# Kernel tuning notes

Hardware: AMD Instinct MI355X
Metric: run time of the kernel (lower is better)

The kernel has to match this reference:

```python
import jax, jax.numpy as jnp
import numpy as np
from jax import lax

K = 5          # CARAFE kernel_size
S = 2          # scale_factor (downsample stride)
GROUP = 1      # mask groups
ENC_PAD = 1    # (encoder_kernel-1)*dilation//2 with encoder_kernel=3


def _conv2d(x, w, b, stride, padding, dilation=1):
    y = lax.conv_general_dilated(
        x, w, window_strides=(stride, stride),
        padding=[(padding, padding), (padding, padding)],
        rhs_dilation=(dilation, dilation),
        dimension_numbers=('NCHW', 'OIHW', 'NCHW'))
    return y + b[None, :, None, None]


def setup_inputs() -> dict:
    key = jax.random.key(0)
    k1, k2, k3 = jax.random.split(key, 3)
    B, C, H, W = 4, 256, 128, 128
    COMP = 64
    x = jax.random.normal(k1, (B, C, H, W), dtype=jnp.float32)
    # xavier-uniform-ish scale for compressor, std=0.001 for content encoder (as in init_weights)
    w1 = jax.random.normal(k2, (COMP, C, 1, 1), dtype=jnp.float32) * (1.0 / np.sqrt(C))
    b1 = jnp.zeros((COMP,), dtype=jnp.float32)
    w2 = jax.random.normal(k3, (K * K * GROUP, COMP, 3, 3), dtype=jnp.float32) * 0.001
    b2 = jnp.zeros((K * K * GROUP,), dtype=jnp.float32)
    return {"x": x, "w1": w1, "b1": b1, "w2": w2, "b2": b2}


def _carafe_forward(x, w1, b1, w2, b2):
    B, C, H, W = x.shape
    compressed = _conv2d(x, w1, b1, stride=1, padding=0)           # (B, 64, H, W)
    mask = _conv2d(compressed, w2, b2, stride=S, padding=ENC_PAD)   # (B, K*K*G, Ho, Wo)
    Ho, Wo = mask.shape[2], mask.shape[3]
    # kernel_normalizer: softmax over the K*K window per group
    mask = jax.nn.softmax(mask.reshape(B, GROUP, K * K, Ho, Wo), axis=2)
    # feature_reassemble: fused unfold * mask sum — accumulate per kernel tap to
    # avoid materializing the full (B, C, K*K, Ho, Wo) tensor.
    pad = K // 2
    x_pad = jnp.pad(x, ((0, 0), (0, 0), (pad, pad), (pad, pad)))
    Cg = C // GROUP
    out = jnp.zeros((B, GROUP, Cg, Ho, Wo), dtype=x.dtype)
    for i in range(K):
        for j in range(K):
            patch = x_pad[:, :, i:i + S * (Ho - 1) + 1:S, j:j + S * (Wo - 1) + 1:S]
            patch = patch.reshape(B, GROUP, Cg, Ho, Wo)
            out = out + patch * mask[:, :, i * K + j][:, :, None]
    return out.reshape(B, C, Ho, Wo)


def reference(x, w1, b1, w2, b2):
    return _carafe_forward(x, w1, b1, w2, b2)
```

## Files before the change

### kernel.cpp

```cpp
#include <hip/hip_runtime.h>
#include <math.h>

#define BN   4
#define CN   256
#define HN   128
#define WN   128
#define COMP 64
#define KK   25
#define HO   64
#define WO   64

#define TB_OFF    36864
#define WS_NEED   ((size_t)(TB_OFF + 256) * 4)

typedef short v8s  __attribute__((ext_vector_type(8)));
typedef float v16f __attribute__((ext_vector_type(16)));

__device__ inline ushort f2bf(float f) {
  unsigned u = __float_as_uint(f);
  return (ushort)((u + 0x7fffu + ((u >> 16) & 1u)) >> 16);
}

__global__ __launch_bounds__(256) void compose_kernel(
    const float* __restrict__ w1, const float* __restrict__ b1,
    const float* __restrict__ w2, float* __restrict__ ws) {
  const int cid = blockIdx.x;
  const int tid = threadIdx.x;
  const int t = cid >> 2;
  const int chunk = (cid & 3) * 4 + (tid >> 6);
  const int lane = tid & 63;
  const int m = lane & 31, half = lane >> 5;
  const int c0 = chunk * 16 + half * 8;
  float acc[8] = {0.f, 0.f, 0.f, 0.f, 0.f, 0.f, 0.f, 0.f};
  if (m < KK) {
    for (int k = 0; k < COMP; ++k) {
      float wv = w2[(size_t)(m * COMP + k) * 9 + t];
      const float* w1r = w1 + (size_t)k * CN + c0;
      float4 a = *(const float4*)w1r;
      float4 bq = *(const float4*)(w1r + 4);
      acc[0] += wv * a.x;  acc[1] += wv * a.y;
      acc[2] += wv * a.z;  acc[3] += wv * a.w;
      acc[4] += wv * bq.x; acc[5] += wv * bq.y;
      acc[6] += wv * bq.z; acc[7] += wv * bq.w;
    }
  }
  ushort* wA = (ushort*)ws;
  ushort pk[8];
#pragma unroll
  for (int j = 0; j < 8; ++j) pk[j] = f2bf(acc[j]);
  *(ushort4*)(wA + ((size_t)(t * 16 + chunk) * 64 + lane) * 8) =
      make_ushort4(pk[0], pk[1], pk[2], pk[3]);
  *(ushort4*)(wA + ((size_t)(t * 16 + chunk) * 64 + lane) * 8 + 4) =
      make_ushort4(pk[4], pk[5], pk[6], pk[7]);
  if (chunk == 0 && lane < KK) {
    float tbv = 0.f;
    for (int k = 0; k < COMP; ++k)
      tbv += w2[(size_t)(lane * COMP + k) * 9 + t] * b1[k];
    ws[TB_OFF + lane * 9 + t] = tbv;
  }
}

__global__ __launch_bounds__(1024, 4) void fused_main(
    const float* __restrict__ ws, const float* __restrict__ b2,
    const float* __restrict__ x, float* __restrict__ out) {
  const int ho = blockIdx.x, b = blockIdx.y;
  const int tid = threadIdx.x;
  const int lane = tid & 63;
  const int wv = tid >> 6;
  const int n = lane & 31, half = lane >> 5;

  __shared__ __attribute__((aligned(16))) char smem[57600];
  float* red = (float*)smem;
  float* sml = (float*)(smem + 51200);

  const ushort* wA = (const ushort*)ws;
  const float* __restrict__ xb = x + (size_t)(b * CN) * (HN * WN);

  const int px = tid & 127;
  const int cg = tid >> 7;
  float sreg[3][8];

  auto stage_load = [&](int c) {
#pragma unroll
    for (int dr = 0; dr < 3; ++dr) {
      const int r = 2 * ho + dr - 1;
      if (r >= 0) {
        const float* xp = xb + ((size_t)(c * 64 + cg * 8) * HN + r) * WN + px;
#pragma unroll
        for (int i = 0; i < 8; ++i) sreg[dr][i] = xp[(size_t)i * (HN * WN)];
      } else {
#pragma unroll
        for (int i = 0; i < 8; ++i) sreg[dr][i] = 0.f;
      }
    }
  };
  auto stage_write = [&]() {
#pragma unroll
    for (int dr = 0; dr < 3; ++dr) {
      v8s o;
#pragma unroll
      for (int i = 0; i < 8; ++i) o[i] = (short)f2bf(sreg[dr][i]);
      const int boff = (((dr * 128 + px) * 64 + cg * 8) * 2)
                       ^ (((px >> 1) & 7) << 4);
      *(v8s*)(smem + boff) = o;
    }
  };

  const int kf = wv & 3;
  const int tg = wv >> 2;
  const v8s zero8 = {};
  v16f acc[2] = {{}, {}};

  stage_load(0);
  for (int c = 0; c < 4; ++c) {
    __syncthreads();
    stage_write();
    __syncthreads();
    if (c < 3) stage_load(c + 1);
    const int kidx = c * 4 + kf;
#pragma unroll
    for (int t = 0; t < 9; ++t) {
      const int tgt = (t >= 6) ? 3 : (t >> 1);
      if (tgt != tg) continue;
      const int dr = t / 3, dc = t % 3;
      if (2 * ho + dr - 1 < 0) continue;
      const v8s af = *(const v8s*)(wA + ((size_t)(t * 16 + kidx) * 64 + lane) * 8);
#pragma unroll
      for (int wt = 0; wt < 2; ++wt) {
        const int q = 2 * (wt * 32 + n) + dc - 1;
        const bool bad = q < 0;
        const int qc = bad ? 0 : q;
        const int boff = (((dr * 128 + qc) * 64 + kf * 16 + half * 8) * 2)
                         ^ (((qc >> 1) & 7) << 4);
        v8s bf = *(const v8s*)(smem + boff);
        if (dc == 0 && bad) bf = zero8;
        acc[wt] = __builtin_amdgcn_mfma_f32_32x32x16_bf16(af, bf, acc[wt], 0, 0, 0);
      }
    }
  }

  const int wo = lane;
  const int c_base = __builtin_amdgcn_readfirstlane(wv * 16);
  const int col = 2 * wo;
  float2 g[2][5];
  auto load_g = [&](int ci, float2* dst) {
    const float* xc = xb + (size_t)(c_base + ci) * (HN * WN);
#pragma unroll
    for (int i = 0; i < 5; ++i) {
      int r = 2 * ho - 2 + i;
      dst[i] = (r >= 0 && r < HN) ? *(const float2*)(xc + r * WN + col)
                                  : make_float2(0.f, 0.f);
    }
  };
  load_g(0, g[0]);
  load_g(1, g[1]);

  __syncthreads();

  if (wv >= 8) {
#pragma unroll
    for (int wt = 0; wt < 2; ++wt)
#pragma unroll
      for (int rg = 0; rg < 16; ++rg) {
        int m = (rg & 3) + 8 * (rg >> 2) + 4 * half;
        if (m < KK) red[((wv - 8) * KK + m) * 64 + wt * 32 + n] = acc[wt][rg];
      }
  }
  __syncthreads();
  if (wv < 8) {
#pragma unroll
    for (int wt = 0; wt < 2; ++wt)
#pragma unroll
      for (int rg = 0; rg < 16; ++rg) {
        int m = (rg & 3) + 8 * (rg >> 2) + 4 * half;
        if (m < KK) red[(wv * KK + m) * 64 + wt * 32 + n] += acc[wt][rg];
      }
  }
  __syncthreads();
  if (wv < 4) {
#pragma unroll
    for (int m = 0; m < KK; ++m)
      red[(wv * KK + m) * 64 + wo] += red[((wv + 4) * KK + m) * 64 + wo];
  }
  __syncthreads();
  if (wv < 2) {
#pragma unroll
    for (int m = 0; m < KK; ++m)
      red[(wv * KK + m) * 64 + wo] += red[((wv + 2) * KK + m) * 64 + wo];
  }
  __syncthreads();
  if (tid < 64) {
    const float* tb = ws + TB_OFF;
    const float vr0 = (ho > 0) ? 1.f : 0.f;
    const float vq0 = (wo > 0) ? 1.f : 0.f;
    float logit[KK];
    float mx = -1e30f;
#pragma unroll
    for (int m = 0; m < KK; ++m) {
      const float* t9 = tb + m * 9;
      float l = b2[m]
              + vr0 * (vq0 * t9[0] + t9[1] + t9[2])
              +       (vq0 * t9[3] + t9[4] + t9[5])
              +       (vq0 * t9[6] + t9[7] + t9[8]);
      l += red[(0 * KK + m) * 64 + wo] + red[(1 * KK + m) * 64 + wo];
      logit[m] = l;
      mx = fmaxf(mx, l);
    }
    float ssum = 0.f;
#pragma unroll
    for (int m = 0; m < KK; ++m) {
      float e = __expf(logit[m] - mx);
      logit[m] = e;
      ssum += e;
    }
    float inv = 1.f / ssum;
#pragma unroll
    for (int m = 0; m < KK; ++m) sml[m * 64 + wo] = logit[m] * inv;
  }
  __syncthreads();

  float smr[KK];
#pragma unroll
  for (int m = 0; m < KK; ++m) smr[m] = sml[m * 64 + wo];

  const float wok = (wo > 0) ? 1.f : 0.f;
  const float w63 = (wo < 63) ? 1.f : 0.f;
  for (int ci = 0; ci < 16; ++ci) {
    float2 v[5];
#pragma unroll
    for (int i = 0; i < 5; ++i) v[i] = g[ci & 1][i];
    if (ci + 2 < 16) load_g(ci + 2, g[ci & 1]);

    float acc2 = 0.f;
#pragma unroll
    for (int i = 0; i < 5; ++i) {
      float lx = wok * __shfl_up(v[i].x, 1, 64);
      float ly = wok * __shfl_up(v[i].y, 1, 64);
      float rx = w63 * __shfl_down(v[i].x, 1, 64);
      acc2 += lx * smr[i * 5 + 0] + ly * smr[i * 5 + 1]
            + v[i].x * smr[i * 5 + 2] + v[i].y * smr[i * 5 + 3]
            + rx * smr[i * 5 + 4];
    }
    out[(((size_t)(b * CN + c_base + ci)) * HO + ho) * WO + wo] = acc2;
  }
}

#define FB_WSTRIDE 240
#define FB_TB_OFF  (256 * FB_WSTRIDE)

__global__ __launch_bounds__(256) void compose_w_fb(
    const float* __restrict__ w1, const float* __restrict__ b1,
    const float* __restrict__ w2, float* __restrict__ ws) {
  int mt = blockIdx.x, c = threadIdx.x;
  float acc = 0.f;
#pragma unroll 8
  for (int k = 0; k < COMP; ++k)
    acc += w2[(size_t)(mt / 9 * COMP + k) * 9 + (mt % 9)] * w1[k * CN + c];
  ws[c * FB_WSTRIDE + mt] = acc;
  if (mt < FB_WSTRIDE - 225) ws[c * FB_WSTRIDE + 225 + mt] = 0.f;
  if (c == 0) {
    float tbv = 0.f;
    for (int k = 0; k < COMP; ++k)
      tbv += w2[(size_t)(mt / 9 * COMP + k) * 9 + (mt % 9)] * b1[k];
    ws[FB_TB_OFF + mt] = tbv;
  }
}

__global__ __launch_bounds__(1024, 4) void fused_fb(
    const float* __restrict__ x, const float* __restrict__ b2,
    const float* __restrict__ ws, float* __restrict__ out) {
  const int ho = blockIdx.x, b = blockIdx.y, tid = threadIdx.x;
  const int wo = tid & 63, wv = tid >> 6;
  const int c_base = __builtin_amdgcn_readfirstlane(wv * 16);
  const float* __restrict__ w2c = ws;
  const float* __restrict__ tb  = ws + FB_TB_OFF;
  __shared__ float red[8 * KK * 64];
  __shared__ float sm[KK * 64];
  const float* __restrict__ xb = x + (size_t)(b * CN) * (HN * WN);
  const int col = 2 * wo;
  float acc[KK];
#pragma unroll
  for (int m = 0; m < KK; ++m) acc[m] = 0.f;
  float2 xbuf[2][3];
  auto load_ch = [&](int ci, float2* dst) {
    const float* xc = xb + (size_t)(c_base + ci) * (HN * WN);
    dst[0] = (ho > 0) ? *(const float2*)(xc + (2 * ho - 1) * WN + col)
                      : make_float2(0.f, 0.f);
    dst[1] = *(const float2*)(xc + (2 * ho) * WN + col);
    dst[2] = *(const float2*)(xc + (2 * ho + 1) * WN + col);
  };
  load_ch(0, xbuf[0]);
  load_ch(1, xbuf[1]);
  const float wok = (wo > 0) ? 1.f : 0.f;
  for (int ci = 0; ci < 16; ++ci) {
    float2 r0 = xbuf[ci & 1][0], r1 = xbuf[ci & 1][1], r2 = xbuf[ci & 1][2];
    if (ci + 2 < 16) load_ch(ci + 2, xbuf[ci & 1]);
    float xv[9];
    xv[0] = wok * __shfl_up(r0.y, 1, 64); xv[1] = r0.x; xv[2] = r0.y;
    xv[3] = wok * __shfl_up(r1.y, 1, 64); xv[4] = r1.x; xv[5] = r1.y;
    xv[6] = wok * __shfl_up(r2.y, 1, 64); xv[7] = r2.x; xv[8] = r2.y;
    const float* __restrict__ wrow = w2c + (size_t)(c_base + ci) * FB_WSTRIDE;
#pragma unroll
    for (int m = 0; m < KK; ++m) {
      float a = acc[m];
#pragma unroll
      for (int t = 0; t < 9; ++t) a += wrow[m * 9 + t] * xv[t];
      acc[m] = a;
    }
  }
  float2 g[2][5];
  auto load_g = [&](int ci, float2* dst) {
    const float* xc = xb + (size_t)(c_base + ci) * (HN * WN);
#pragma unroll
    for (int i = 0; i < 5; ++i) {
      int r = 2 * ho - 2 + i;
      dst[i] = (r >= 0 && r < HN) ? *(const float2*)(xc + r * WN + col)
                                  : make_float2(0.f, 0.f);
    }
  };
  load_g(0, g[0]);
  load_g(1, g[1]);
  if (wv >= 8) {
#pragma unroll
    for (int m = 0; m < KK; ++m) red[((wv - 8) * KK + m) * 64 + wo] = acc[m];
  }
  __syncthreads();
  if (wv < 8) {
#pragma unroll
    for (int m = 0; m < KK; ++m) red[(wv * KK + m) * 64 + wo] += acc[m];
  }
  __syncthreads();
  if (wv < 4) {
#pragma unroll
    for (int m = 0; m < KK; ++m)
      red[(wv * KK + m) * 64 + wo] += red[((wv + 4) * KK + m) * 64 + wo];
  }
  __syncthreads();
  if (wv < 2) {
#pragma unroll
    for (int m = 0; m < KK; ++m)
      red[(wv * KK + m) * 64 + wo] += red[((wv + 2) * KK + m) * 64 + wo];
  }
  __syncthreads();
  if (tid < 64) {
    const float vr0 = (ho > 0) ? 1.f : 0.f;
    const float vq0 = (wo > 0) ? 1.f : 0.f;
    float logit[KK];
    float mx = -1e30f;
#pragma unroll
    for (int m = 0; m < KK; ++m) {
      const float* t9 = tb + m * 9;
      float l = b2[m]
              + vr0 * (vq0 * t9[0] + t9[1] + t9[2])
              +       (vq0 * t9[3] + t9[4] + t9[5])
              +       (vq0 * t9[6] + t9[7] + t9[8]);
      l += red[(0 * KK + m) * 64 + wo] + red[(1 * KK + m) * 64 + wo];
      logit[m] = l;
      mx = fmaxf(mx, l);
    }
    float s = 0.f;
#pragma unroll
    for (int m = 0; m < KK; ++m) {
      float e = __expf(logit[m] - mx);
      logit[m] = e;
      s += e;
    }
    float inv = 1.f / s;
#pragma unroll
    for (int m = 0; m < KK; ++m) sm[m * 64 + wo] = logit[m] * inv;
  }
  __syncthreads();
  float smr[KK];
#pragma unroll
  for (int m = 0; m < KK; ++m) smr[m] = sm[m * 64 + wo];
  const float w63 = (wo < 63) ? 1.f : 0.f;
  for (int ci = 0; ci < 16; ++ci) {
    float2 v[5];
#pragma unroll
    for (int i = 0; i < 5; ++i) v[i] = g[ci & 1][i];
    if (ci + 2 < 16) load_g(ci + 2, g[ci & 1]);
    float acc2 = 0.f;
#pragma unroll
    for (int i = 0; i < 5; ++i) {
      float lx = wok * __shfl_up(v[i].x, 1, 64);
      float ly = wok * __shfl_up(v[i].y, 1, 64);
      float rx = w63 * __shfl_down(v[i].x, 1, 64);
      acc2 += lx * smr[i * 5 + 0] + ly * smr[i * 5 + 1]
            + v[i].x * smr[i * 5 + 2] + v[i].y * smr[i * 5 + 3]
            + rx * smr[i * 5 + 4];
    }
    out[(((size_t)(b * CN + c_base + ci)) * HO + ho) * WO + wo] = acc2;
  }
}

extern "C" void kernel_launch(void* const* d_in, const int* in_sizes, int n_in,
                              void* d_out, int out_size, void* d_ws, size_t ws_size,
                              hipStream_t stream) {
  const float* x  = (const float*)d_in[0];
  const float* w1 = (const float*)d_in[1];
  const float* b1 = (const float*)d_in[2];
  const float* w2 = (const float*)d_in[3];
  const float* b2 = (const float*)d_in[4];
  float* out = (float*)d_out;
  float* ws  = (float*)d_ws;

  if (ws_size >= WS_NEED) {
    hipLaunchKernelGGL(compose_kernel, dim3(36), dim3(256), 0, stream,
                       w1, b1, w2, ws);
    hipLaunchKernelGGL(fused_main, dim3(HO, BN), dim3(1024), 0, stream,
                       ws, b2, x, out);
  } else {
    hipLaunchKernelGGL(compose_w_fb, dim3(225), dim3(256), 0, stream,
                       w1, b1, w2, ws);
    hipLaunchKernelGGL(fused_fb, dim3(HO, BN), dim3(1024), 0, stream,
                       x, b2, ws, out);
  }
}
```

Before: 149.0 us.

## Split fused CARAFE kernel into channel-split conv partials and softmax-gather kernel

The single fused kernel, which ran 256 blocks each looping over four channel chunks, becomes two kernels. The first computes per-chunk partial mask logits across a 4x larger grid and writes them to workspace. The second sums the four partials, applies softmax, and reassembles a quarter of the output channels per block. This raises block count and occupancy and removes the serial channel loop. In exchange it adds a global round-trip for partial logits, an extra launch, and redundant softmax work in each of the four channel-quarter blocks.

```diff
diff --git a/kernel.cpp b/kernel.cpp
--- a/kernel.cpp
+++ b/kernel.cpp
@@ -11,7 +11,9 @@
 #define WO   64
 
 #define TB_OFF    36864
-#define WS_NEED   ((size_t)(TB_OFF + 256) * 4)
+#define P_OFF     37120
+#define P_COUNT   ((size_t)BN * HO * 4 * KK * 64)
+#define WS_NEED   ((size_t)(P_OFF + P_COUNT) * 4)
 
 typedef short v8s  __attribute__((ext_vector_type(8)));
 typedef float v16f __attribute__((ext_vector_type(16)));
@@ -60,18 +62,16 @@
   }
 }
 
-__global__ __launch_bounds__(1024, 4) void fused_main(
-    const float* __restrict__ ws, const float* __restrict__ b2,
-    const float* __restrict__ x, float* __restrict__ out) {
-  const int ho = blockIdx.x, b = blockIdx.y;
+__global__ __launch_bounds__(1024, 8) void conv_partial(
+    float* __restrict__ ws, const float* __restrict__ x) {
+  const int ho = blockIdx.x, b = blockIdx.y, cq = blockIdx.z;
   const int tid = threadIdx.x;
   const int lane = tid & 63;
   const int wv = tid >> 6;
   const int n = lane & 31, half = lane >> 5;
 
-  __shared__ __attribute__((aligned(16))) char smem[57600];
+  __shared__ __attribute__((aligned(16))) char smem[51200];
   float* red = (float*)smem;
-  float* sml = (float*)(smem + 51200);
 
   const ushort* wA = (const ushort*)ws;
   const float* __restrict__ xb = x + (size_t)(b * CN) * (HN * WN);
@@ -79,68 +79,109 @@
   const int px = tid & 127;
   const int cg = tid >> 7;
   float sreg[3][8];
-
-  auto stage_load = [&](int c) {
-#pragma unroll
-    for (int dr = 0; dr < 3; ++dr) {
-      const int r = 2 * ho + dr - 1;
-      if (r >= 0) {
-        const float* xp = xb + ((size_t)(c * 64 + cg * 8) * HN + r) * WN + px;
-#pragma unroll
-        for (int i = 0; i < 8; ++i) sreg[dr][i] = xp[(size_t)i * (HN * WN)];
-      } else {
-#pragma unroll
-        for (int i = 0; i < 8; ++i) sreg[dr][i] = 0.f;
-      }
-    }
-  };
-  auto stage_write = [&]() {
-#pragma unroll
-    for (int dr = 0; dr < 3; ++dr) {
-      v8s o;
-#pragma unroll
-      for (int i = 0; i < 8; ++i) o[i] = (short)f2bf(sreg[dr][i]);
-      const int boff = (((dr * 128 + px) * 64 + cg * 8) * 2)
-                       ^ (((px >> 1) & 7) << 4);
-      *(v8s*)(smem + boff) = o;
-    }
-  };
+#pragma unroll
+  for (int dr = 0; dr < 3; ++dr) {
+    const int r = 2 * ho + dr - 1;
+    if (r >= 0) {
+      const float* xp = xb + ((size_t)(cq * 64 + cg * 8) * HN + r) * WN + px;
+#pragma unroll
+      for (int i = 0; i < 8; ++i) sreg[dr][i] = xp[(size_t)i * (HN * WN)];
+    } else {
+#pragma unroll
+      for (int i = 0; i < 8; ++i) sreg[dr][i] = 0.f;
+    }
+  }
+#pragma unroll
+  for (int dr = 0; dr < 3; ++dr) {
+    v8s o;
+#pragma unroll
+    for (int i = 0; i < 8; ++i) o[i] = (short)f2bf(sreg[dr][i]);
+    const int boff = (((dr * 128 + px) * 64 + cg * 8) * 2)
+                     ^ (((px >> 1) & 7) << 4);
+    *(v8s*)(smem + boff) = o;
+  }
+  __syncthreads();
 
   const int kf = wv & 3;
   const int tg = wv >> 2;
+  const int kidx = cq * 4 + kf;
   const v8s zero8 = {};
   v16f acc[2] = {{}, {}};
-
-  stage_load(0);
-  for (int c = 0; c < 4; ++c) {
-    __syncthreads();
-    stage_write();
-    __syncthreads();
-    if (c < 3) stage_load(c + 1);
-    const int kidx = c * 4 + kf;
-#pragma unroll
-    for (int t = 0; t < 9; ++t) {
-      const int tgt = (t >= 6) ? 3 : (t >> 1);
-      if (tgt != tg) continue;
-      const int dr = t / 3, dc = t % 3;
-      if (2 * ho + dr - 1 < 0) continue;
-      const v8s af = *(const v8s*)(wA + ((size_t)(t * 16 + kidx) * 64 + lane) * 8);
-#pragma unroll
-      for (int wt = 0; wt < 2; ++wt) {
-        const int q = 2 * (wt * 32 + n) + dc - 1;
-        const bool bad = q < 0;
-        const int qc = bad ? 0 : q;
-        const int boff = (((dr * 128 + qc) * 64 + kf * 16 + half * 8) * 2)
-                         ^ (((qc >> 1) & 7) << 4);
-        v8s bf = *(const v8s*)(smem + boff);
-        if (dc == 0 && bad) bf = zero8;
-        acc[wt] = __builtin_amdgcn_mfma_f32_32x32x16_bf16(af, bf, acc[wt], 0, 0, 0);
+#pragma unroll
+  for (int t = 0; t < 9; ++t) {
+    const int tgt = (t >= 6) ? 3 : (t >> 1);
+    if (tgt != tg) continue;
+    const int dr = t / 3, dc = t % 3;
+    if (2 * ho + dr - 1 < 0) continue;
+    const v8s af = *(const v8s*)(wA + ((size_t)(t * 16 + kidx) * 64 + lane) * 8);
+#pragma unroll
+    for (int wt = 0; wt < 2; ++wt) {
+      const int q = 2 * (wt * 32 + n) + dc - 1;
+      const bool bad = q < 0;
+      const int qc = bad ? 0 : q;
+      const int boff = (((dr * 128 + qc) * 64 + kf * 16 + half * 8) * 2)
+                       ^ (((qc >> 1) & 7) << 4);
+      v8s bf = *(const v8s*)(smem + boff);
+      if (dc == 0 && bad) bf = zero8;
+      acc[wt] = __builtin_amdgcn_mfma_f32_32x32x16_bf16(af, bf, acc[wt], 0, 0, 0);
+    }
+  }
+  __syncthreads();
+
+  if (wv >= 8) {
+#pragma unroll
+    for (int wt = 0; wt < 2; ++wt)
+#pragma unroll
+      for (int rg = 0; rg < 16; ++rg) {
+        int m = (rg & 3) + 8 * (rg >> 2) + 4 * half;
+        if (m < KK) red[((wv - 8) * KK + m) * 64 + wt * 32 + n] = acc[wt][rg];
       }
-    }
-  }
-
+  }
+  __syncthreads();
+  if (wv < 8) {
+#pragma unroll
+    for (int wt = 0; wt < 2; ++wt)
+#pragma unroll
+      for (int rg = 0; rg < 16; ++rg) {
+        int m = (rg & 3) + 8 * (rg >> 2) + 4 * half;
+        if (m < KK) red[(wv * KK + m) * 64 + wt * 32 + n] += acc[wt][rg];
+      }
+  }
+  __syncthreads();
+  if (wv < 4) {
+#pragma unroll
+    for (int m = 0; m < KK; ++m)
+      red[(wv * KK + m) * 64 + lane] += red[((wv + 4) * KK + m) * 64 + lane];
+  }
+  __syncthreads();
+  if (wv < 2) {
+#pragma unroll
+    for (int m = 0; m < KK; ++m)
+      red[(wv * KK + m) * 64 + lane] += red[((wv + 2) * KK + m) * 64 + lane];
+  }
+  __syncthreads();
+  if (tid < 64) {
+    float* P = ws + P_OFF + (size_t)(((b * HO + ho) * 4 + cq) * KK) * 64;
+#pragma unroll
+    for (int m = 0; m < KK; ++m)
+      P[m * 64 + lane] =
+          red[(0 * KK + m) * 64 + lane] + red[(1 * KK + m) * 64 + lane];
+  }
+}
+
+__global__ __launch_bounds__(1024, 8) void softmax_gather(
+    const float* __restrict__ ws, const float* __restrict__ b2,
+    const float* __restrict__ x, float* __restrict__ out) {
+  const int ho = blockIdx.x, b = blockIdx.y, cq = blockIdx.z;
+  const int tid = threadIdx.x;
+  const int lane = tid & 63;
+  const int wv = tid >> 6;
+
+  __shared__ float sml[KK * 64];
+
+  const float* __restrict__ xb = x + (size_t)(b * CN) * (HN * WN);
   const int wo = lane;
-  const int c_base = __builtin_amdgcn_readfirstlane(wv * 16);
+  const int c_base = __builtin_amdgcn_readfirstlane(cq * 64 + wv * 4);
   const int col = 2 * wo;
   float2 g[2][5];
   auto load_g = [&](int ci, float2* dst) {
@@ -155,42 +196,9 @@
   load_g(0, g[0]);
   load_g(1, g[1]);
 
-  __syncthreads();
-
-  if (wv >= 8) {
-#pragma unroll
-    for (int wt = 0; wt < 2; ++wt)
-#pragma unroll
-      for (int rg = 0; rg < 16; ++rg) {
-        int m = (rg & 3) + 8 * (rg >> 2) + 4 * half;
-        if (m < KK) red[((wv - 8) * KK + m) * 64 + wt * 32 + n] = acc[wt][rg];
-      }
-  }
-  __syncthreads();
-  if (wv < 8) {
-#pragma unroll
-    for (int wt = 0; wt < 2; ++wt)
-#pragma unroll
-      for (int rg = 0; rg < 16; ++rg) {
-        int m = (rg & 3) + 8 * (rg >> 2) + 4 * half;
-        if (m < KK) red[(wv * KK + m) * 64 + wt * 32 + n] += acc[wt][rg];
-      }
-  }
-  __syncthreads();
-  if (wv < 4) {
-#pragma unroll
-    for (int m = 0; m < KK; ++m)
-      red[(wv * KK + m) * 64 + wo] += red[((wv + 4) * KK + m) * 64 + wo];
-  }
-  __syncthreads();
-  if (wv < 2) {
-#pragma unroll
-    for (int m = 0; m < KK; ++m)
-      red[(wv * KK + m) * 64 + wo] += red[((wv + 2) * KK + m) * 64 + wo];
-  }
-  __syncthreads();
   if (tid < 64) {
     const float* tb = ws + TB_OFF;
+    const float* P = ws + P_OFF + (size_t)((b * HO + ho) * 4) * KK * 64;
     const float vr0 = (ho > 0) ? 1.f : 0.f;
     const float vq0 = (wo > 0) ? 1.f : 0.f;
     float logit[KK];
@@ -202,7 +210,8 @@
               + vr0 * (vq0 * t9[0] + t9[1] + t9[2])
               +       (vq0 * t9[3] + t9[4] + t9[5])
               +       (vq0 * t9[6] + t9[7] + t9[8]);
-      l += red[(0 * KK + m) * 64 + wo] + red[(1 * KK + m) * 64 + wo];
+      l += P[(0 * KK + m) * 64 + wo] + P[(1 * KK + m) * 64 + wo]
+         + P[(2 * KK + m) * 64 + wo] + P[(3 * KK + m) * 64 + wo];
       logit[m] = l;
       mx = fmaxf(mx, l);
     }
@@ -225,11 +234,11 @@
 
   const float wok = (wo > 0) ? 1.f : 0.f;
   const float w63 = (wo < 63) ? 1.f : 0.f;
-  for (int ci = 0; ci < 16; ++ci) {
+  for (int ci = 0; ci < 4; ++ci) {
     float2 v[5];
 #pragma unroll
     for (int i = 0; i < 5; ++i) v[i] = g[ci & 1][i];
-    if (ci + 2 < 16) load_g(ci + 2, g[ci & 1]);
+    if (ci + 2 < 4) load_g(ci + 2, g[ci & 1]);
 
     float acc2 = 0.f;
 #pragma unroll
@@ -407,7 +416,9 @@
   if (ws_size >= WS_NEED) {
     hipLaunchKernelGGL(compose_kernel, dim3(36), dim3(256), 0, stream,
                        w1, b1, w2, ws);
-    hipLaunchKernelGGL(fused_main, dim3(HO, BN), dim3(1024), 0, stream,
+    hipLaunchKernelGGL(conv_partial, dim3(HO, BN, 4), dim3(1024), 0, stream,
+                       ws, x);
+    hipLaunchKernelGGL(softmax_gather, dim3(HO, BN, 4), dim3(1024), 0, stream,
                        ws, b2, x, out);
   } else {
     hipLaunchKernelGGL(compose_w_fb, dim3(225), dim3(256), 0, stream,
```

Measured after the change: 194.2 us. +30.3%, slower.

## Split each output row across two blocks by width half with halo exchange

Applied to the files above, without the earlier changes.

The main fused kernel now launches a third grid dimension so each block handles only 32 of the 64 output columns. The compressed-input staging covers a 72-pixel window with a 4-pixel halo instead of the full 128-pixel row. Each wave now runs one MFMA tile instead of two, and the A fragments are loaded before the barrier. Halo values for the reassembly shuffles at the half boundary are staged in LDS. The goal is to double the block count, raising occupancy and parallelism on the 256-CU device, and to shrink LDS use. The cost is redundant halo loads and a more complex edge handling at the split.

```diff
diff --git a/kernel.cpp b/kernel.cpp
--- a/kernel.cpp
+++ b/kernel.cpp
@@ -60,32 +60,39 @@
   }
 }
 
-__global__ __launch_bounds__(1024, 4) void fused_main(
+#define SML_OFF 27648
+#define EL_OFF  30848
+#define ER_OFF  41088
+#define LDS_SZ  46208
+
+__global__ __launch_bounds__(1024, 4) void fused_half(
     const float* __restrict__ ws, const float* __restrict__ b2,
     const float* __restrict__ x, float* __restrict__ out) {
-  const int ho = blockIdx.x, b = blockIdx.y;
+  const int ho = blockIdx.x, b = blockIdx.y, h = blockIdx.z;
   const int tid = threadIdx.x;
   const int lane = tid & 63;
   const int wv = tid >> 6;
   const int n = lane & 31, half = lane >> 5;
 
-  __shared__ __attribute__((aligned(16))) char smem[57600];
+  __shared__ __attribute__((aligned(16))) char smem[LDS_SZ];
   float* red = (float*)smem;
-  float* sml = (float*)(smem + 51200);
+  float* sml = (float*)(smem + SML_OFF);
 
   const ushort* wA = (const ushort*)ws;
   const float* __restrict__ xb = x + (size_t)(b * CN) * (HN * WN);
 
-  const int px = tid & 127;
+  const int p = tid & 127;
   const int cg = tid >> 7;
+  const int q = 64 * h - 4 + p;
+  const bool pok = (p < 72) && (q >= 0) && (q < WN);
   float sreg[3][8];
 
   auto stage_load = [&](int c) {
 #pragma unroll
     for (int dr = 0; dr < 3; ++dr) {
       const int r = 2 * ho + dr - 1;
-      if (r >= 0) {
-        const float* xp = xb + ((size_t)(c * 64 + cg * 8) * HN + r) * WN + px;
+      if (pok && r >= 0) {
+        const float* xp = xb + ((size_t)(c * 64 + cg * 8) * HN + r) * WN + q;
 #pragma unroll
         for (int i = 0; i < 8; ++i) sreg[dr][i] = xp[(size_t)i * (HN * WN)];
       } else {
@@ -95,104 +102,125 @@
     }
   };
   auto stage_write = [&]() {
-#pragma unroll
-    for (int dr = 0; dr < 3; ++dr) {
-      v8s o;
-#pragma unroll
-      for (int i = 0; i < 8; ++i) o[i] = (short)f2bf(sreg[dr][i]);
-      const int boff = (((dr * 128 + px) * 64 + cg * 8) * 2)
-                       ^ (((px >> 1) & 7) << 4);
-      *(v8s*)(smem + boff) = o;
+    if (p < 72) {
+#pragma unroll
+      for (int dr = 0; dr < 3; ++dr) {
+        v8s o;
+#pragma unroll
+        for (int i = 0; i < 8; ++i) o[i] = (short)f2bf(sreg[dr][i]);
+        const int boff = (((dr * 72 + p) * 64 + cg * 8) * 2)
+                         ^ (((p >> 1) & 7) << 4);
+        *(v8s*)(smem + boff) = o;
+      }
     }
   };
 
   const int kf = wv & 3;
   const int tg = wv >> 2;
-  const v8s zero8 = {};
-  v16f acc[2] = {{}, {}};
+  const int t0 = (tg < 3) ? 2 * tg : 6;
+  const int ntap = (tg < 3) ? 2 : 3;
+  v16f acc = {};
 
   stage_load(0);
   for (int c = 0; c < 4; ++c) {
     __syncthreads();
     stage_write();
+    const int kidx = c * 4 + kf;
+    v8s afr[3];
+#pragma unroll
+    for (int tt = 0; tt < 3; ++tt)
+      if (tt < ntap)
+        afr[tt] = *(const v8s*)(wA + ((size_t)((t0 + tt) * 16 + kidx) * 64 + lane) * 8);
     __syncthreads();
     if (c < 3) stage_load(c + 1);
-    const int kidx = c * 4 + kf;
-#pragma unroll
-    for (int t = 0; t < 9; ++t) {
-      const int tgt = (t >= 6) ? 3 : (t >> 1);
-      if (tgt != tg) continue;
+#pragma unroll
+    for (int tt = 0; tt < 3; ++tt) {
+      if (tt >= ntap) continue;
+      const int t = t0 + tt;
       const int dr = t / 3, dc = t % 3;
       if (2 * ho + dr - 1 < 0) continue;
-      const v8s af = *(const v8s*)(wA + ((size_t)(t * 16 + kidx) * 64 + lane) * 8);
-#pragma unroll
-      for (int wt = 0; wt < 2; ++wt) {
-        const int q = 2 * (wt * 32 + n) + dc - 1;
-        const bool bad = q < 0;
-        const int qc = bad ? 0 : q;
-        const int boff = (((dr * 128 + qc) * 64 + kf * 16 + half * 8) * 2)
-                         ^ (((qc >> 1) & 7) << 4);
-        v8s bf = *(const v8s*)(smem + boff);
-        if (dc == 0 && bad) bf = zero8;
-        acc[wt] = __builtin_amdgcn_mfma_f32_32x32x16_bf16(af, bf, acc[wt], 0, 0, 0);
-      }
-    }
-  }
-
-  const int wo = lane;
-  const int c_base = __builtin_amdgcn_readfirstlane(wv * 16);
-  const int col = 2 * wo;
+      const int pb = 2 * n + dc + 3;
+      const int boff = (((dr * 72 + pb) * 64 + kf * 16 + half * 8) * 2)
+                       ^ (((pb >> 1) & 7) << 4);
+      v8s bf = *(const v8s*)(smem + boff);
+      acc = __builtin_amdgcn_mfma_f32_32x32x16_bf16(afr[tt], bf, acc, 0, 0, 0);
+    }
+  }
+
+  const int lo = n;
+  const int oc = 32 * h + lo;
+  const int colb = 64 * h + 2 * lo;
   float2 g[2][5];
   auto load_g = [&](int ci, float2* dst) {
-    const float* xc = xb + (size_t)(c_base + ci) * (HN * WN);
+    const float* xc = xb + (size_t)(wv * 16 + half * 8 + ci) * (HN * WN);
 #pragma unroll
     for (int i = 0; i < 5; ++i) {
       int r = 2 * ho - 2 + i;
-      dst[i] = (r >= 0 && r < HN) ? *(const float2*)(xc + r * WN + col)
+      dst[i] = (r >= 0 && r < HN) ? *(const float2*)(xc + r * WN + colb)
                                   : make_float2(0.f, 0.f);
     }
   };
   load_g(0, g[0]);
   load_g(1, g[1]);
 
+  {
+    float* eLf = (float*)(smem + EL_OFF);
+    float* eRf = (float*)(smem + ER_OFF);
+#pragma unroll
+    for (int it = 0; it < 2; ++it) {
+      const int idx = it * 1024 + tid;
+      const int ch = idx >> 3, sl = idx & 7;
+      if (sl < 5) {
+        const int r = 2 * ho - 2 + sl;
+        float2 lv = make_float2(0.f, 0.f);
+        float rv = 0.f;
+        if (r >= 0 && r < HN) {
+          const float* xc = xb + (size_t)ch * (HN * WN) + (size_t)r * WN;
+          if (h == 1) lv = *(const float2*)(xc + 62);
+          else        rv = xc[64];
+        }
+        *(float2*)(eLf + (ch * 5 + sl) * 2) = lv;
+        eRf[ch * 5 + sl] = rv;
+      }
+    }
+  }
+
   __syncthreads();
 
   if (wv >= 8) {
 #pragma unroll
-    for (int wt = 0; wt < 2; ++wt)
-#pragma unroll
-      for (int rg = 0; rg < 16; ++rg) {
-        int m = (rg & 3) + 8 * (rg >> 2) + 4 * half;
-        if (m < KK) red[((wv - 8) * KK + m) * 64 + wt * 32 + n] = acc[wt][rg];
-      }
+    for (int rg = 0; rg < 16; ++rg) {
+      int m = (rg & 3) + 8 * (rg >> 2) + 4 * half;
+      if (m < KK) red[((wv - 8) * KK + m) * 32 + n] = acc[rg];
+    }
   }
   __syncthreads();
   if (wv < 8) {
 #pragma unroll
-    for (int wt = 0; wt < 2; ++wt)
-#pragma unroll
-      for (int rg = 0; rg < 16; ++rg) {
-        int m = (rg & 3) + 8 * (rg >> 2) + 4 * half;
-        if (m < KK) red[(wv * KK + m) * 64 + wt * 32 + n] += acc[wt][rg];
-      }
+    for (int rg = 0; rg < 16; ++rg) {
+      int m = (rg & 3) + 8 * (rg >> 2) + 4 * half;
+      if (m < KK) red[(wv * KK + m) * 32 + n] += acc[rg];
+    }
   }
   __syncthreads();
   if (wv < 4) {
-#pragma unroll
-    for (int m = 0; m < KK; ++m)
-      red[(wv * KK + m) * 64 + wo] += red[((wv + 4) * KK + m) * 64 + wo];
+#pragma unroll 13
+    for (int m = half; m < KK; m += 2)
+      red[(wv * KK + m) * 32 + n] += red[((wv + 4) * KK + m) * 32 + n];
   }
   __syncthreads();
   if (wv < 2) {
-#pragma unroll
-    for (int m = 0; m < KK; ++m)
-      red[(wv * KK + m) * 64 + wo] += red[((wv + 2) * KK + m) * 64 + wo];
-  }
-  __syncthreads();
-  if (tid < 64) {
+#pragma unroll 13
+    for (int m = half; m < KK; m += 2)
+      red[(wv * KK + m) * 32 + n] += red[((wv + 2) * KK + m) * 32 + n];
+  }
+  __syncthreads();
+  if (tid < 32) {
     const float* tb = ws + TB_OFF;
+    const int wo32 = tid;
+    const int occ = 32 * h + wo32;
     const float vr0 = (ho > 0) ? 1.f : 0.f;
-    const float vq0 = (wo > 0) ? 1.f : 0.f;
+    const float vq0 = (occ > 0) ? 1.f : 0.f;
     float logit[KK];
     float mx = -1e30f;
 #pragma unroll
@@ -202,7 +230,7 @@
               + vr0 * (vq0 * t9[0] + t9[1] + t9[2])
               +       (vq0 * t9[3] + t9[4] + t9[5])
               +       (vq0 * t9[6] + t9[7] + t9[8]);
-      l += red[(0 * KK + m) * 64 + wo] + red[(1 * KK + m) * 64 + wo];
+      l += red[(0 * KK + m) * 32 + wo32] + red[(1 * KK + m) * 32 + wo32];
       logit[m] = l;
       mx = fmaxf(mx, l);
     }
@@ -215,33 +243,41 @@
     }
     float inv = 1.f / ssum;
 #pragma unroll
-    for (int m = 0; m < KK; ++m) sml[m * 64 + wo] = logit[m] * inv;
+    for (int m = 0; m < KK; ++m) sml[m * 32 + wo32] = logit[m] * inv;
   }
   __syncthreads();
 
   float smr[KK];
 #pragma unroll
-  for (int m = 0; m < KK; ++m) smr[m] = sml[m * 64 + wo];
-
-  const float wok = (wo > 0) ? 1.f : 0.f;
-  const float w63 = (wo < 63) ? 1.f : 0.f;
-  for (int ci = 0; ci < 16; ++ci) {
+  for (int m = 0; m < KK; ++m) smr[m] = sml[m * 32 + lo];
+
+  const float* eLf = (const float*)(smem + EL_OFF);
+  const float* eRf = (const float*)(smem + ER_OFF);
+  const float wok = (oc > 0) ? 1.f : 0.f;
+  const float w63 = (oc < 63) ? 1.f : 0.f;
+#pragma unroll
+  for (int ci = 0; ci < 8; ++ci) {
+    const int ch = wv * 16 + half * 8 + ci;
     float2 v[5];
 #pragma unroll
     for (int i = 0; i < 5; ++i) v[i] = g[ci & 1][i];
-    if (ci + 2 < 16) load_g(ci + 2, g[ci & 1]);
+    if (ci + 2 < 8) load_g(ci + 2, g[ci & 1]);
 
     float acc2 = 0.f;
 #pragma unroll
     for (int i = 0; i < 5; ++i) {
-      float lx = wok * __shfl_up(v[i].x, 1, 64);
-      float ly = wok * __shfl_up(v[i].y, 1, 64);
-      float rx = w63 * __shfl_down(v[i].x, 1, 64);
-      acc2 += lx * smr[i * 5 + 0] + ly * smr[i * 5 + 1]
+      const float2 elv = *(const float2*)(eLf + (ch * 5 + i) * 2);
+      const float erv = eRf[ch * 5 + i];
+      float lxs = __shfl_up(v[i].x, 1, 32);
+      float lys = __shfl_up(v[i].y, 1, 32);
+      float rxs = __shfl_down(v[i].x, 1, 32);
+      if (lo == 0)  { lxs = elv.x; lys = elv.y; }
+      if (lo == 31) { rxs = erv; }
+      acc2 += wok * (lxs * smr[i * 5 + 0] + lys * smr[i * 5 + 1])
             + v[i].x * smr[i * 5 + 2] + v[i].y * smr[i * 5 + 3]
-            + rx * smr[i * 5 + 4];
-    }
-    out[(((size_t)(b * CN + c_base + ci)) * HO + ho) * WO + wo] = acc2;
+            + w63 * rxs * smr[i * 5 + 4];
+    }
+    out[(((size_t)(b * CN + ch)) * HO + ho) * WO + oc] = acc2;
   }
 }
 
@@ -407,7 +443,7 @@
   if (ws_size >= WS_NEED) {
     hipLaunchKernelGGL(compose_kernel, dim3(36), dim3(256), 0, stream,
                        w1, b1, w2, ws);
-    hipLaunchKernelGGL(fused_main, dim3(HO, BN), dim3(1024), 0, stream,
+    hipLaunchKernelGGL(fused_half, dim3(HO, BN, 2), dim3(1024), 0, stream,
                        ws, b2, x, out);
   } else {
     hipLaunchKernelGGL(compose_w_fb, dim3(225), dim3(256), 0, stream,
```

Measured after the change: 167.1 us. 12.1% more time.
